# Performance work log

Measured on AMD Instinct MI355X. Metric: run time of the kernel, lower is better.

Reference implementation:

```python
import jax, jax.numpy as jnp
import numpy as np

N, LC, LQ, D = 16, 2048, 256, 256  # D = 2 * LSTM_HIDDEN_DIM


def setup_inputs() -> dict:
    key = jax.random.key(0)
    k1, k2, k3 = jax.random.split(key, 3)
    emb_context = jax.random.normal(k1, (N, LC, D), dtype=jnp.float32)
    emb_query = jax.random.normal(k2, (N, LQ, D), dtype=jnp.float32)
    # Linear(6H=3D, 1, bias=False) weight, flattened to (3D,)
    W = jax.random.normal(k3, (3 * D,), dtype=jnp.float32) / np.sqrt(3 * D)
    return {"emb_context": emb_context, "emb_query": emb_query, "W": W}


def reference(emb_context, emb_query, W):
    d = emb_context.shape[-1]
    # Algebraic decomposition of the expand+cat+linear similarity score:
    # S[n,i,j] = c_i . w_c + q_j . w_q + sum_d c_i[d]*q_j[d]*w_m[d]
    w_c, w_q, w_m = W[:d], W[d:2 * d], W[2 * d:]
    S = (
        jnp.einsum('ncd,d->nc', emb_context, w_c)[:, :, None]
        + jnp.einsum('nqd,d->nq', emb_query, w_q)[:, None, :]
        + jnp.einsum('ncd,nqd->ncq', emb_context * w_m, emb_query)
    )  # (N, Lc, Lq)
    # context-to-query attention
    c2q_attn = jnp.einsum('ncq,nqd->ncd', jax.nn.softmax(S, axis=-1), emb_query)
    # query-to-context attention (max over query dim, softmax over context dim)
    b = jax.nn.softmax(jnp.max(S, axis=2), axis=-1)  # (N, Lc)
    q2c_attn = jnp.einsum('nc,ncd->nd', b, emb_context)[:, None, :]  # (N, 1, D), broadcasts over Lc
    G = jnp.concatenate(
        [emb_context, c2q_attn, emb_context * c2q_attn, emb_context * q2c_attn],
        axis=2,
    )  # (N, Lc, 4D) == (N, Lc, 8*LSTM_HIDDEN_DIM)
    return G
```

## Files before the change

### kernel.cpp

```cpp
#include <hip/hip_runtime.h>
#include <math.h>

#define BN 16
#define LC 2048
#define LQ 256
#define DD 256
#define BM 128
#define NT 512

typedef _Float16 half8 __attribute__((ext_vector_type(8)));
typedef float f32x16 __attribute__((ext_vector_type(16)));

typedef const __attribute__((address_space(1))) void* gas_p;
typedef __attribute__((address_space(3))) void* lds_p;
#define GLOAD_LDS16(gp, lp) \
    __builtin_amdgcn_global_load_lds((gas_p)(gp), (lds_p)(lp), 16, 0, 0)

__device__ __forceinline__ float waveReduceSum(float v) {
#pragma unroll
    for (int o = 32; o > 0; o >>= 1) v += __shfl_xor(v, o, 64);
    return v;
}
__device__ __forceinline__ float waveReduceMax(float v) {
#pragma unroll
    for (int o = 32; o > 0; o >>= 1) v = fmaxf(v, __shfl_xor(v, o, 64));
    return v;
}

__global__ __launch_bounds__(256) void k_prep(const float* __restrict__ q,
                                              const float* __restrict__ W,
                                              _Float16* __restrict__ Qh,
                                              _Float16* __restrict__ QTh,
                                              float* __restrict__ cq) {
    __shared__ float tile[32][257];
    const int n = blockIdx.y;
    const int q0 = blockIdx.x * 32;
    const int t = threadIdx.x;

#pragma unroll
    for (int i = 0; i < 32; ++i) {
        const float v = q[((size_t)(n * LQ + q0 + i)) * DD + t];
        Qh[((size_t)(n * LQ + q0 + i)) * DD + t] = (_Float16)v;
        tile[i][t] = v;
    }
    __syncthreads();

    {
        const int row = t >> 3, sub = t & 7;
        float s = 0.f;
#pragma unroll
        for (int j = 0; j < 32; ++j)
            s = fmaf(tile[row][sub * 32 + j], W[DD + sub * 32 + j], s);
        s += __shfl_xor(s, 1, 64);
        s += __shfl_xor(s, 2, 64);
        s += __shfl_xor(s, 4, 64);
        if (sub == 0) cq[n * LQ + q0 + row] = s;
    }

    const int tx = t & 31, ty = t >> 5;
#pragma unroll
    for (int db = 0; db < 8; ++db) {
#pragma unroll
        for (int i = 0; i < 4; ++i) {
            const int d = db * 32 + ty + 8 * i;
            QTh[((size_t)(n * DD + d)) * LQ + q0 + tx] = (_Float16)tile[tx][d];
        }
    }
}

__global__ __launch_bounds__(NT) void k_main(const float* __restrict__ ctx,
                                             const _Float16* __restrict__ Qh,
                                             const _Float16* __restrict__ QTh,
                                             const float* __restrict__ cq,
                                             const float* __restrict__ W,
                                             float* __restrict__ out,
                                             float* __restrict__ pq,
                                             float* __restrict__ KS) {
    __shared__ _Float16 Abuf[BM * 256];
    __shared__ _Float16 Bbuf[2][256 * 64];
    __shared__ float rowterm[BM];
    __shared__ float m_lds[BM];
    __shared__ float linv_lds[BM];
    __shared__ float eexp[BM];
    __shared__ float redmax[4][BM];
    __shared__ float redsum[4][BM];

    const int t = threadIdx.x;
    const int lane = t & 63, wid = t >> 6;
    const int l31 = lane & 31, lh = lane >> 5;
    const int wr = wid >> 2, wc = wid & 3;
    const int blk = blockIdx.x;
    const int n = blk >> 4;
    const int blk16 = blk & 15;
    const int c0 = blk16 * BM;

    const _Float16* Qhn = Qh + (size_t)n * LQ * DD;
    const _Float16* QThn = QTh + (size_t)n * DD * LQ;

    auto stageB = [&](int kc, const _Float16* src, int buf) {
#pragma unroll
        for (int j = 0; j < 4; ++j) {
            const int r = wid * 32 + j * 8 + (lane >> 3);
            const int gs = (lane & 7) ^ (r & 7);
            const _Float16* gp = src + (size_t)r * 256 + kc * 64 + gs * 8;
            _Float16* lp = &Bbuf[buf][(wid * 32 + j * 8) * 64];
            GLOAD_LDS16(gp, lp);
        }
    };

    auto gemmChunk = [&](f32x16 (&acc)[2][2], int kcA, int buf) {
#pragma unroll
        for (int kk = 0; kk < 4; ++kk) {
            half8 af[2], bf[2];
#pragma unroll
            for (int mt = 0; mt < 2; ++mt) {
                const int row = 64 * wr + 32 * mt + l31;
                const int kb = kcA * 128 + 32 * kk + 16 * lh;
                af[mt] = *(const half8*)((const char*)Abuf + row * 512 + (kb ^ ((row & 7) << 4)));
            }
#pragma unroll
            for (int nt = 0; nt < 2; ++nt) {
                const int row = 64 * wc + 32 * nt + l31;
                const int kb = 32 * kk + 16 * lh;
                bf[nt] = *(const half8*)((const char*)Bbuf[buf] + row * 128 + (kb ^ ((row & 7) << 4)));
            }
#pragma unroll
            for (int mt = 0; mt < 2; ++mt)
#pragma unroll
                for (int nt = 0; nt < 2; ++nt)
                    acc[mt][nt] = __builtin_amdgcn_mfma_f32_32x32x16_f16(af[mt], bf[nt], acc[mt][nt], 0, 0, 0);
        }
    };

    stageB(0, Qhn, 0);

    {
        const int g = t & 31;
        const int r0 = t >> 5;
        float wmv[8], wcv[8];
#pragma unroll
        for (int j = 0; j < 8; ++j) {
            wmv[j] = W[2 * DD + g * 8 + j];
            wcv[j] = W[g * 8 + j];
        }
#pragma unroll
        for (int i = 0; i < 8; ++i) {
            const int r = r0 + 16 * i;
            const float* srcr = ctx + ((size_t)(n * LC + c0 + r)) * DD + g * 8;
            const float4 aa = *(const float4*)srcr;
            const float4 bb = *(const float4*)(srcr + 4);
            const float vals[8] = {aa.x, aa.y, aa.z, aa.w, bb.x, bb.y, bb.z, bb.w};
            half8 cmv;
            float rt = 0.f;
#pragma unroll
            for (int j = 0; j < 8; ++j) {
                cmv[j] = (_Float16)(vals[j] * wmv[j]);
                rt = fmaf(vals[j], wcv[j], rt);
            }
            *(half8*)((char*)Abuf + r * 512 + ((g * 16) ^ ((r & 7) << 4))) = cmv;
#pragma unroll
            for (int o = 16; o > 0; o >>= 1) rt += __shfl_xor(rt, o, 64);
            if (g == 0) rowterm[r] = rt;
        }
    }
    __syncthreads();

    f32x16 acc[2][2] = {};
#pragma unroll
    for (int kc = 0; kc < 4; ++kc) {
        if (kc) __syncthreads();
        if (kc < 3) stageB(kc + 1, Qhn, (kc + 1) & 1);
        else stageB(0, QThn, 0);
        gemmChunk(acc, kc, kc & 1);
    }
    __syncthreads();

    float cqv[2];
    cqv[0] = cq[n * LQ + 64 * wc + l31];
    cqv[1] = cq[n * LQ + 64 * wc + 32 + l31];

#pragma unroll
    for (int mt = 0; mt < 2; ++mt) {
#pragma unroll
        for (int r = 0; r < 16; ++r) {
            const int rl = 64 * wr + 32 * mt + (r & 3) + 8 * (r >> 2) + 4 * lh;
            const float rterm = rowterm[rl];
            const float v0 = acc[mt][0][r] + rterm + cqv[0];
            const float v1 = acc[mt][1][r] + rterm + cqv[1];
            acc[mt][0][r] = v0;
            acc[mt][1][r] = v1;
            float mx = fmaxf(v0, v1);
#pragma unroll
            for (int o = 16; o > 0; o >>= 1) mx = fmaxf(mx, __shfl_xor(mx, o, 64));
            if (l31 == 0) redmax[wc][rl] = mx;
        }
    }
    __syncthreads();
    if (t < BM)
        m_lds[t] = fmaxf(fmaxf(redmax[0][t], redmax[1][t]), fmaxf(redmax[2][t], redmax[3][t]));
    __syncthreads();

    if (t < BM) {
        const float mv = m_lds[t];
        const float kb = waveReduceMax(mv);
        const float e = __expf(mv - kb);
        eexp[t] = e;
        const float sb = waveReduceSum(e);
        if (lane == 0) {
            KS[(n * 32 + blk16 * 2 + (t >> 6)) * 2 + 0] = kb;
            KS[(n * 32 + blk16 * 2 + (t >> 6)) * 2 + 1] = sb;
        }
    }

#pragma unroll
    for (int mt = 0; mt < 2; ++mt) {
#pragma unroll
        for (int r = 0; r < 16; ++r) {
            const int rl = 64 * wr + 32 * mt + (r & 3) + 8 * (r >> 2) + 4 * lh;
            const float mrow = m_lds[rl];
            const float p0 = __expf(acc[mt][0][r] - mrow);
            const float p1 = __expf(acc[mt][1][r] - mrow);
            const int q0 = 64 * wc + l31, q1 = q0 + 32;
            *((_Float16*)((char*)Abuf + rl * 512 + ((q0 * 2) ^ ((rl & 7) << 4)))) = (_Float16)p0;
            *((_Float16*)((char*)Abuf + rl * 512 + ((q1 * 2) ^ ((rl & 7) << 4)))) = (_Float16)p1;
            float sm = p0 + p1;
#pragma unroll
            for (int o = 16; o > 0; o >>= 1) sm += __shfl_xor(sm, o, 64);
            if (l31 == 0) redsum[wc][rl] = sm;
        }
    }
    __syncthreads();
    if (t < BM)
        linv_lds[t] = 1.0f / (redsum[0][t] + redsum[1][t] + redsum[2][t] + redsum[3][t]);
    __syncthreads();

    f32x16 acc2[2][2] = {};
#pragma unroll
    for (int kc = 0; kc < 4; ++kc) {
        if (kc) __syncthreads();
        if (kc < 3) stageB(kc + 1, QThn, (kc + 1) & 1);
        gemmChunk(acc2, kc, kc & 1);
    }

    float pqa[2] = {0.f, 0.f};
#pragma unroll
    for (int mt = 0; mt < 2; ++mt) {
#pragma unroll
        for (int nt = 0; nt < 2; ++nt) {
            const int col = 64 * wc + 32 * nt + l31;
#pragma unroll
            for (int r = 0; r < 16; ++r) {
                const int rl = 64 * wr + 32 * mt + (r & 3) + 8 * (r >> 2) + 4 * lh;
                const size_t gc = (size_t)(n * LC + c0 + rl);
                const float li = linv_lds[rl];
                const float ctxv = ctx[gc * DD + col];
                const float ov = acc2[mt][nt][r] * li;
                const size_t ob = gc * 1024 + col;
                out[ob] = ctxv;
                out[ob + 256] = ov;
                out[ob + 512] = ctxv * ov;
                pqa[nt] = fmaf(eexp[rl], ctxv, pqa[nt]);
            }
        }
    }
#pragma unroll
    for (int nt = 0; nt < 2; ++nt) {
        pqa[nt] += __shfl_xor(pqa[nt], 32, 64);
        if (lh == 0) {
            const int col = 64 * wc + 32 * nt + l31;
            pq[((size_t)(n * 32 + blk16 * 2 + wr)) * 256 + col] = pqa[nt];
        }
    }
}

__global__ __launch_bounds__(256) void k_tail(const float* __restrict__ ctx,
                                              const float* __restrict__ pq,
                                              const float* __restrict__ KS,
                                              float* __restrict__ out) {
    const int blk = blockIdx.x;
    const int n = blk >> 5;
    const int c0 = (blk & 31) * 64;
    const int t = threadIdx.x;

    float bmax = -1e30f;
#pragma unroll
    for (int b = 0; b < 32; ++b) bmax = fmaxf(bmax, KS[(n * 32 + b) * 2]);
    float Z = 0.f;
    float acc = 0.f;
#pragma unroll
    for (int b = 0; b < 32; ++b) {
        const float w = __expf(KS[(n * 32 + b) * 2] - bmax);
        Z = fmaf(w, KS[(n * 32 + b) * 2 + 1], Z);
        acc = fmaf(w, pq[((size_t)(n * 32 + b)) * 256 + t], acc);
    }
    const float q2cd = acc / Z;

#pragma unroll 4
    for (int r = 0; r < 64; ++r) {
        const size_t gc = (size_t)(n * LC + c0 + r);
        out[gc * 1024 + 768 + t] = ctx[gc * DD + t] * q2cd;
    }
}

extern "C" void kernel_launch(void* const* d_in, const int* in_sizes, int n_in,
                              void* d_out, int out_size, void* d_ws, size_t ws_size,
                              hipStream_t stream) {
    const float* ctx = (const float*)d_in[0];
    const float* q = (const float*)d_in[1];
    const float* W = (const float*)d_in[2];
    float* out = (float*)d_out;

    _Float16* Qh = (_Float16*)d_ws;
    _Float16* QTh = Qh + (size_t)BN * LQ * DD;
    float* fws = (float*)(QTh + (size_t)BN * DD * LQ);
    float* cq = fws;
    float* pq = cq + BN * LQ;
    float* KS = pq + BN * 32 * 256;

    k_prep<<<dim3(LQ / 32, BN), 256, 0, stream>>>(q, W, Qh, QTh, cq);
    k_main<<<BN * LC / BM, NT, 0, stream>>>(ctx, Qh, QTh, cq, W, out, pq, KS);
    k_tail<<<BN * LC / 64, 256, 0, stream>>>(ctx, pq, KS, out);
}
```

Baseline: 70.64 us.

## Fuse q2c tail into main kernel via cooperative grid sync

```diff
diff --git a/kernel.cpp b/kernel.cpp
--- a/kernel.cpp
+++ b/kernel.cpp
@@ -1,5 +1,8 @@
 #include <hip/hip_runtime.h>
+#include <hip/hip_cooperative_groups.h>
 #include <math.h>
+
+namespace cg = cooperative_groups;
 
 #define BN 16
 #define LC 2048
@@ -68,14 +71,14 @@
     }
 }
 
-__global__ __launch_bounds__(NT) void k_main(const float* __restrict__ ctx,
-                                             const _Float16* __restrict__ Qh,
-                                             const _Float16* __restrict__ QTh,
-                                             const float* __restrict__ cq,
-                                             const float* __restrict__ W,
-                                             float* __restrict__ out,
-                                             float* __restrict__ pq,
-                                             float* __restrict__ KS) {
+__global__ __launch_bounds__(NT, 2) void k_fused(const float* __restrict__ ctx,
+                                                 const _Float16* __restrict__ Qh,
+                                                 const _Float16* __restrict__ QTh,
+                                                 const float* __restrict__ cq,
+                                                 const float* __restrict__ W,
+                                                 float* __restrict__ out,
+                                                 float* __restrict__ pq,
+                                                 float* __restrict__ KS) {
     __shared__ _Float16 Abuf[BM * 256];
     __shared__ _Float16 Bbuf[2][256 * 64];
     __shared__ float rowterm[BM];
@@ -242,6 +245,7 @@
         gemmChunk(acc2, kc, kc & 1);
     }
 
+    float ctxv[2][2][16];
     float pqa[2] = {0.f, 0.f};
 #pragma unroll
     for (int mt = 0; mt < 2; ++mt) {
@@ -253,13 +257,14 @@
                 const int rl = 64 * wr + 32 * mt + (r & 3) + 8 * (r >> 2) + 4 * lh;
                 const size_t gc = (size_t)(n * LC + c0 + rl);
                 const float li = linv_lds[rl];
-                const float ctxv = ctx[gc * DD + col];
+                const float cv = ctx[gc * DD + col];
+                ctxv[mt][nt][r] = cv;
                 const float ov = acc2[mt][nt][r] * li;
                 const size_t ob = gc * 1024 + col;
-                out[ob] = ctxv;
+                out[ob] = cv;
                 out[ob + 256] = ov;
-                out[ob + 512] = ctxv * ov;
-                pqa[nt] = fmaf(eexp[rl], ctxv, pqa[nt]);
+                out[ob + 512] = cv * ov;
+                pqa[nt] = fmaf(eexp[rl], cv, pqa[nt]);
             }
         }
     }
@@ -271,34 +276,36 @@
             pq[((size_t)(n * 32 + blk16 * 2 + wr)) * 256 + col] = pqa[nt];
         }
     }
-}
-
-__global__ __launch_bounds__(256) void k_tail(const float* __restrict__ ctx,
-                                              const float* __restrict__ pq,
-                                              const float* __restrict__ KS,
-                                              float* __restrict__ out) {
-    const int blk = blockIdx.x;
-    const int n = blk >> 5;
-    const int c0 = (blk & 31) * 64;
-    const int t = threadIdx.x;
-
+
+    __threadfence();
+    cg::this_grid().sync();
+    __threadfence();
+
+    const int col0 = 64 * wc + l31;
+    const int col1 = col0 + 32;
     float bmax = -1e30f;
 #pragma unroll
     for (int b = 0; b < 32; ++b) bmax = fmaxf(bmax, KS[(n * 32 + b) * 2]);
-    float Z = 0.f;
-    float acc = 0.f;
+    float Z = 0.f, a0 = 0.f, a1 = 0.f;
 #pragma unroll
     for (int b = 0; b < 32; ++b) {
         const float w = __expf(KS[(n * 32 + b) * 2] - bmax);
         Z = fmaf(w, KS[(n * 32 + b) * 2 + 1], Z);
-        acc = fmaf(w, pq[((size_t)(n * 32 + b)) * 256 + t], acc);
-    }
-    const float q2cd = acc / Z;
-
-#pragma unroll 4
-    for (int r = 0; r < 64; ++r) {
-        const size_t gc = (size_t)(n * LC + c0 + r);
-        out[gc * 1024 + 768 + t] = ctx[gc * DD + t] * q2cd;
+        a0 = fmaf(w, pq[((size_t)(n * 32 + b)) * 256 + col0], a0);
+        a1 = fmaf(w, pq[((size_t)(n * 32 + b)) * 256 + col1], a1);
+    }
+    const float zi = 1.0f / Z;
+    const float q2c0 = a0 * zi, q2c1 = a1 * zi;
+
+#pragma unroll
+    for (int mt = 0; mt < 2; ++mt) {
+#pragma unroll
+        for (int r = 0; r < 16; ++r) {
+            const int rl = 64 * wr + 32 * mt + (r & 3) + 8 * (r >> 2) + 4 * lh;
+            const size_t ob = ((size_t)(n * LC + c0 + rl)) * 1024 + 768;
+            out[ob + col0] = ctxv[mt][0][r] * q2c0;
+            out[ob + col1] = ctxv[mt][1][r] * q2c1;
+        }
     }
 }
 
@@ -318,6 +325,9 @@
     float* KS = pq + BN * 32 * 256;
 
     k_prep<<<dim3(LQ / 32, BN), 256, 0, stream>>>(q, W, Qh, QTh, cq);
-    k_main<<<BN * LC / BM, NT, 0, stream>>>(ctx, Qh, QTh, cq, W, out, pq, KS);
-    k_tail<<<BN * LC / 64, 256, 0, stream>>>(ctx, pq, KS, out);
-}
+
+    void* args[] = {(void*)&ctx, (void*)&Qh, (void*)&QTh, (void*)&cq,
+                    (void*)&W, (void*)&out, (void*)&pq, (void*)&KS};
+    hipLaunchCooperativeKernel((void*)k_fused, dim3(BN * LC / BM), dim3(NT),
+                               args, 0, stream);
+}
```

Result: slower. 207.8 us (+194.2%).
